# Kernel tuning notes

Hardware: AMD Instinct MI355X
Metric: run time of the kernel (lower is better)

The kernel has to match this reference:

```python
import jax, jax.numpy as jnp
import numpy as np

TOP_K = 2
CAP_FACTOR = 1.25


def _gelu(x):
    # custom tanh GELU matching the torch module
    return 0.5 * x * (1.0 + jnp.tanh(jnp.sqrt(2.0 / jnp.pi) * (x + 0.044715 * x ** 3)))


def setup_inputs() -> dict:
    key = jax.random.key(0)
    ks = jax.random.split(key, 6)
    B, S, D, F, E = 4, 2048, 1024, 4096, 8
    return {
        "hidden_states": jax.random.normal(ks[0], (B, S, D), dtype=jnp.float32),
        "wr": jax.random.normal(ks[1], (E, D), dtype=jnp.float32) * 0.02,  # router weight (Linear, no bias)
        "w1": jax.random.normal(ks[2], (E, D, F), dtype=jnp.float32) * 0.02,
        "b1": jnp.zeros((E, F), dtype=jnp.float32),
        "w2": jax.random.normal(ks[3], (E, F, D), dtype=jnp.float32) * 0.02,
        "b2": jnp.zeros((E, D), dtype=jnp.float32),
    }


def reference(hidden_states, wr, w1, b1, w2, b2):
    B, S, D = hidden_states.shape
    E = wr.shape[0]
    x = hidden_states.reshape(-1, D)  # [T, D]
    T = x.shape[0]

    # ---- router (eval mode: no noise) ----
    logits = x @ wr.T  # [T, E]
    vals, idx = jax.lax.top_k(logits, TOP_K)  # [T, K]
    sparse = jnp.full((T, E), -jnp.inf, dtype=logits.dtype)
    sparse = sparse.at[jnp.arange(T)[:, None], idx].set(vals)
    gating = jax.nn.softmax(sparse, axis=-1)  # [T, E], zero off top-k

    # ---- capacity-limited dispatch ----
    cap = max(8, int(max(1, T * TOP_K // E) * CAP_FACTOR))
    mask = (idx[:, :, None] == jnp.arange(E)).any(axis=1)  # [T, E]
    pos = jnp.cumsum(mask.astype(jnp.int32), axis=0) - 1  # rank of token within expert
    keep = mask & (pos < cap)
    slot = jnp.where(keep, pos, cap)  # overflow -> dummy slot
    e_grid = jnp.broadcast_to(jnp.arange(E)[None, :], (T, E))
    t_grid = jnp.broadcast_to(jnp.arange(T)[:, None], (T, E))
    dispatch = jnp.full((E, cap + 1), T, dtype=jnp.int32)
    dispatch = dispatch.at[e_grid, slot].set(t_grid)[:, :cap]  # [E, cap], T = pad

    # ---- grouped expert MLP ----
    x_pad = jnp.concatenate([x, jnp.zeros((1, D), x.dtype)], axis=0)
    g_pad = jnp.concatenate([gating, jnp.zeros((1, E), gating.dtype)], axis=0)
    xg = x_pad[dispatch]  # [E, cap, D]
    h = _gelu(jnp.einsum('ecd,edf->ecf', xg, w1) + b1[:, None, :])
    y = jnp.einsum('ecf,efd->ecd', h, w2) + b2[:, None, :]  # [E, cap, D]
    g = g_pad[dispatch, jnp.arange(E)[:, None]]  # [E, cap]; 0 for padded slots
    wy = y * g[..., None]

    # ---- combine (scatter-add) ----
    out = jax.ops.segment_sum(wy.reshape(-1, D), dispatch.reshape(-1), num_segments=T + 1)[:T]
    return out.reshape(B, S, D)
```

## Files before the change

### kernel.cpp

```cpp
#include <hip/hip_runtime.h>
#include <cstdint>
#include <cstddef>

#define T_TOK 8192
#define D_DIM 1024
#define F_DIM 4096
#define E_NUM 8
#define CAP   2560
#define BKS   32
#define MYB   20
#define LDSB  16384

typedef __attribute__((ext_vector_type(8))) short bf16x8;
typedef __attribute__((ext_vector_type(8))) unsigned short u16x8;
typedef __attribute__((ext_vector_type(4))) float f32x4;

typedef const __attribute__((address_space(1))) void* gas_ptr;
typedef __attribute__((address_space(3))) void* las_ptr;

__device__ __forceinline__ unsigned short f2bf(float f) {
  unsigned u = __float_as_uint(f);
  u += 0x7FFF + ((u >> 16) & 1);
  return (unsigned short)(u >> 16);
}

__device__ __forceinline__ float gelu_f(float x) {
  float u = 0.7978845608028654f * (x + 0.044715f * x * x * x);
  float t = 1.0f - 2.0f / (__expf(2.0f * u) + 1.0f);
  return 0.5f * x * (1.0f + t);
}

__device__ __forceinline__ int xcd_swizzle(int bid, int nwg) {
  int q = nwg >> 3;
  return (bid & 7) * q + (bid >> 3);
}

#define PIPE_BAR4() asm volatile("s_waitcnt vmcnt(4)\n\ts_barrier" ::: "memory")
#define PIPE_BAR0() asm volatile("s_waitcnt vmcnt(0)\n\ts_barrier" ::: "memory")

__global__ __launch_bounds__(256) void route_kernel(
    const float* __restrict__ x, const float* __restrict__ wr,
    unsigned short* __restrict__ xbf, int2* __restrict__ tokE,
    float2* __restrict__ tokG)
{
  int tid = threadIdx.x;
  int l = tid & 63;
  int w = tid >> 6;
  int t = blockIdx.x * 4 + w;
  const float4* xr = (const float4*)(x + (size_t)t * D_DIM);
  ushort4* xbr = (ushort4*)(xbf + (size_t)t * D_DIM);
  float acc[E_NUM];
#pragma unroll
  for (int e = 0; e < E_NUM; ++e) acc[e] = 0.f;
#pragma unroll
  for (int c = 0; c < D_DIM / 256; ++c) {
    float4 xv = xr[c * 64 + l];
    ushort4 bv;
    bv.x = f2bf(xv.x); bv.y = f2bf(xv.y); bv.z = f2bf(xv.z); bv.w = f2bf(xv.w);
    xbr[c * 64 + l] = bv;
#pragma unroll
    for (int e = 0; e < E_NUM; ++e) {
      float4 wv = ((const float4*)(wr + (size_t)e * D_DIM))[c * 64 + l];
      acc[e] += xv.x * wv.x + xv.y * wv.y + xv.z * wv.z + xv.w * wv.w;
    }
  }
#pragma unroll
  for (int e = 0; e < E_NUM; ++e) {
#pragma unroll
    for (int s = 32; s > 0; s >>= 1) acc[e] += __shfl_xor(acc[e], s);
  }
  if (l == 0) {
    int e1 = 0; float v1 = acc[0];
#pragma unroll
    for (int e = 1; e < E_NUM; ++e) if (acc[e] > v1) { v1 = acc[e]; e1 = e; }
    int e2 = -1; float v2 = -3.4e38f;
#pragma unroll
    for (int e = 0; e < E_NUM; ++e) if (e != e1 && acc[e] > v2) { v2 = acc[e]; e2 = e; }
    float s = __expf(v2 - v1);
    float g1 = 1.f / (1.f + s);
    tokE[t] = make_int2(e1, e2);
    tokG[t] = make_float2(g1, s * g1);
  }
}

__global__ __launch_bounds__(256) void scan_kernel(
    const int2* __restrict__ tokE, const float2* __restrict__ tokG,
    int* __restrict__ dispatch, float* __restrict__ sgate, int* __restrict__ cnt)
{
  int e = blockIdx.x;
  int tid = threadIdx.x;
  int l = tid & 63;
  int w = tid >> 6;
  __shared__ int wsum[4];
  int base = 0;
  for (int chunk = 0; chunk < T_TOK; chunk += 256) {
    int t = chunk + tid;
    int2 te = tokE[t];
    float2 tg = tokG[t];
    bool f1 = (te.x == e);
    bool f2 = (te.y == e);
    bool f = f1 || f2;
    unsigned long long m = __ballot(f);
    int rank = __popcll(m & ((1ull << l) - 1ull));
    if (l == 0) wsum[w] = __popcll(m);
    __syncthreads();
    int woff = 0;
#pragma unroll
    for (int i = 0; i < 4; ++i) if (i < w) woff += wsum[i];
    int tot = wsum[0] + wsum[1] + wsum[2] + wsum[3];
    int pos = base + woff + rank;
    if (f && pos < CAP) {
      dispatch[e * CAP + pos] = t;
      sgate[e * CAP + pos] = f1 ? tg.x : tg.y;
    }
    base += tot;
    __syncthreads();
  }
  int start = base < CAP ? base : CAP;
  for (int p = start + tid; p < CAP; p += 256) {
    dispatch[e * CAP + p] = T_TOK;
    sgate[e * CAP + p] = 0.f;
  }
  if (tid == 0) cnt[e] = base < CAP ? base : CAP;
}

__global__ __launch_bounds__(256) void transpose_kernel(
    const float* __restrict__ src, unsigned short* __restrict__ dst,
    int K, int N)
{
  const float* s = src + (size_t)blockIdx.z * K * N;
  unsigned short* d = dst + (size_t)blockIdx.z * K * N;
  __shared__ float tile[64][65];
  int n0 = blockIdx.x * 64;
  int k0 = blockIdx.y * 64;
  int tid = threadIdx.x;
  int r = tid >> 4;
  int c4 = (tid & 15) * 4;
#pragma unroll
  for (int i = 0; i < 4; ++i) {
    int row = r + i * 16;
    float4 v = *(const float4*)&s[(size_t)(k0 + row) * N + n0 + c4];
    tile[row][c4] = v.x; tile[row][c4 + 1] = v.y;
    tile[row][c4 + 2] = v.z; tile[row][c4 + 3] = v.w;
  }
  __syncthreads();
  int n = tid >> 2;
  int kg = tid & 3;
#pragma unroll
  for (int j = 0; j < 2; ++j) {
    int kc = kg * 2 + j;
    u16x8 o;
#pragma unroll
    for (int q = 0; q < 8; ++q) o[q] = f2bf(tile[kc * 8 + q][n]);
    *(u16x8*)&d[(size_t)(n0 + n) * K + k0 + kc * 8] = o;
  }
}


#define G1_NXB (F_DIM / 128)
__global__ __launch_bounds__(256, 3) void gemm1_kernel(
    const unsigned short* __restrict__ xbf,
    const unsigned short* __restrict__ w1t,
    const float* __restrict__ b1,
    const int* __restrict__ dispatch,
    const int* __restrict__ cnt,
    unsigned short* __restrict__ h,
    int e_base, size_t w1stride, size_t hstride)
{
  int wg = xcd_swizzle(blockIdx.x, gridDim.x);
  int my = wg % MYB;
  int p  = wg / MYB;
  int nx = p % G1_NXB;
  int ez = p / G1_NXB;
  int e = e_base + ez;
  int m0 = my * 128;
  if (m0 >= cnt[e]) return;
  const unsigned short* w1e = w1t + (size_t)ez * w1stride;
  unsigned short* he = h + (size_t)ez * hstride;
  int n0 = nx * 128;
  int tid = threadIdx.x;
  int l = tid & 63;
  int wid = tid >> 6;
  int wm = wid >> 1, wn = wid & 1;
  int lrow = l & 15, lhi = l >> 4;

  __shared__ __align__(16) char lds[3 * LDSB];

  const unsigned short* ag[2];
  const unsigned short* bg[2];
  int ldsA[2], ldsB[2];
#pragma unroll
  for (int j = 0; j < 2; ++j) {
    int chunk = wid * 2 + j;
    int U = chunk * 64 + l;
    int u = U ^ ((U >> 3) & 7);
    int row = u >> 2, s = u & 3;
    int tok = dispatch[e * CAP + m0 + row];
    ag[j] = xbf + (size_t)tok * D_DIM + s * 8;
    bg[j] = w1e + (size_t)(n0 + row) * D_DIM + s * 8;
    ldsA[j] = chunk * 1024;
    ldsB[j] = 8192 + chunk * 1024;
  }

  int aoff[4], boff[4];
#pragma unroll
  for (int m = 0; m < 4; ++m) {
    int row = wm * 64 + m * 16 + lrow;
    int u = row * 4 + lhi;
    aoff[m] = (u ^ ((row >> 1) & 7)) * 16;
    int colr = wn * 64 + m * 16 + lrow;
    int ub = colr * 4 + lhi;
    boff[m] = 8192 + (ub ^ ((colr >> 1) & 7)) * 16;
  }

  f32x4 acc[4][4];
#pragma unroll
  for (int m = 0; m < 4; ++m)
#pragma unroll
    for (int n = 0; n < 4; ++n) acc[m][n] = (f32x4){0.f, 0.f, 0.f, 0.f};

#define STAGE1(BASE, KOFF) do { \
    __builtin_amdgcn_global_load_lds((gas_ptr)(ag[0] + (KOFF)), (las_ptr)(lds + (BASE) + ldsA[0]), 16, 0, 0); \
    __builtin_amdgcn_global_load_lds((gas_ptr)(bg[0] + (KOFF)), (las_ptr)(lds + (BASE) + ldsB[0]), 16, 0, 0); \
    __builtin_amdgcn_global_load_lds((gas_ptr)(ag[1] + (KOFF)), (las_ptr)(lds + (BASE) + ldsA[1]), 16, 0, 0); \
    __builtin_amdgcn_global_load_lds((gas_ptr)(bg[1] + (KOFF)), (las_ptr)(lds + (BASE) + ldsB[1]), 16, 0, 0); \
  } while (0)

  const int NT = D_DIM / BKS;
  STAGE1(0, 0);
  STAGE1(LDSB, BKS);
  PIPE_BAR4();

  int cb = 0, sb = 2 * LDSB, koff = 2 * BKS;
  for (int t = 0; t < NT; ++t) {
    if (t + 2 < NT) { STAGE1(sb, koff); koff += BKS; }
    bf16x8 af[4], bfr[4];
#pragma unroll
    for (int m = 0; m < 4; ++m) af[m] = *(const bf16x8*)(lds + cb + aoff[m]);
#pragma unroll
    for (int n = 0; n < 4; ++n) bfr[n] = *(const bf16x8*)(lds + cb + boff[n]);
    __builtin_amdgcn_s_setprio(1);
#pragma unroll
    for (int m = 0; m < 4; ++m)
#pragma unroll
      for (int n = 0; n < 4; ++n)
        acc[m][n] = __builtin_amdgcn_mfma_f32_16x16x32_bf16(af[m], bfr[n], acc[m][n], 0, 0, 0);
    __builtin_amdgcn_s_setprio(0);
    if (t + 1 < NT) {
      if (t + 2 < NT) PIPE_BAR4(); else PIPE_BAR0();
      cb = (cb == 2 * LDSB) ? 0 : cb + LDSB;
      sb = (sb == 2 * LDSB) ? 0 : sb + LDSB;
    }
  }

  int colg[4]; float b1v[4];
#pragma unroll
  for (int n = 0; n < 4; ++n) {
    colg[n] = n0 + wn * 64 + n * 16 + lrow;
    b1v[n] = b1[e * F_DIM + colg[n]];
  }
#pragma unroll
  for (int m = 0; m < 4; ++m) {
    int rb = m0 + wm * 64 + m * 16 + lhi * 4;
#pragma unroll
    for (int j = 0; j < 4; ++j) {
      int r = rb + j;
      unsigned short* hr = he + (size_t)r * F_DIM;
#pragma unroll
      for (int n = 0; n < 4; ++n) {
        float v = acc[m][n][j] + b1v[n];
        hr[colg[n]] = f2bf(gelu_f(v));
      }
    }
  }
}

#define G2_NXB (D_DIM / 128)
__global__ __launch_bounds__(256, 3) void gemm2_kernel(
    const unsigned short* __restrict__ h,
    const unsigned short* __restrict__ w2t,
    const float* __restrict__ b2,
    const int* __restrict__ dispatch,
    const float* __restrict__ sgate,
    const int* __restrict__ cnt,
    float* __restrict__ out,
    int e_base, size_t w2stride, size_t hstride)
{
  int wg = xcd_swizzle(blockIdx.x, gridDim.x);
  int my = wg % MYB;
  int p  = wg / MYB;
  int nx = p % G2_NXB;
  int ez = p / G2_NXB;
  int e = e_base + ez;
  int m0 = my * 128;
  if (m0 >= cnt[e]) return;
  const unsigned short* he = h + (size_t)ez * hstride;
  const unsigned short* w2e = w2t + (size_t)ez * w2stride;
  int n0 = nx * 128;
  int tid = threadIdx.x;
  int l = tid & 63;
  int wid = tid >> 6;
  int wm = wid >> 1, wn = wid & 1;
  int lrow = l & 15, lhi = l >> 4;

  __shared__ __align__(16) char lds[3 * LDSB];

  const unsigned short* ag[2];
  const unsigned short* bg[2];
  int ldsA[2], ldsB[2];
#pragma unroll
  for (int j = 0; j < 2; ++j) {
    int chunk = wid * 2 + j;
    int U = chunk * 64 + l;
    int u = U ^ ((U >> 3) & 7);
    int row = u >> 2, s = u & 3;
    ag[j] = he + (size_t)(m0 + row) * F_DIM + s * 8;
    bg[j] = w2e + (size_t)(n0 + row) * F_DIM + s * 8;
    ldsA[j] = chunk * 1024;
    ldsB[j] = 8192 + chunk * 1024;
  }

  int aoff[4], boff[4];
#pragma unroll
  for (int m = 0; m < 4; ++m) {
    int row = wm * 64 + m * 16 + lrow;
    int u = row * 4 + lhi;
    aoff[m] = (u ^ ((row >> 1) & 7)) * 16;
    int colr = wn * 64 + m * 16 + lrow;
    int ub = colr * 4 + lhi;
    boff[m] = 8192 + (ub ^ ((colr >> 1) & 7)) * 16;
  }

  f32x4 acc[4][4];
#pragma unroll
  for (int m = 0; m < 4; ++m)
#pragma unroll
    for (int n = 0; n < 4; ++n) acc[m][n] = (f32x4){0.f, 0.f, 0.f, 0.f};

#define STAGE2(BASE, KOFF) do { \
    __builtin_amdgcn_global_load_lds((gas_ptr)(ag[0] + (KOFF)), (las_ptr)(lds + (BASE) + ldsA[0]), 16, 0, 0); \
    __builtin_amdgcn_global_load_lds((gas_ptr)(bg[0] + (KOFF)), (las_ptr)(lds + (BASE) + ldsB[0]), 16, 0, 0); \
    __builtin_amdgcn_global_load_lds((gas_ptr)(ag[1] + (KOFF)), (las_ptr)(lds + (BASE) + ldsA[1]), 16, 0, 0); \
    __builtin_amdgcn_global_load_lds((gas_ptr)(bg[1] + (KOFF)), (las_ptr)(lds + (BASE) + ldsB[1]), 16, 0, 0); \
  } while (0)

  const int NT = F_DIM / BKS;
  STAGE2(0, 0);
  STAGE2(LDSB, BKS);
  PIPE_BAR4();

  int cb = 0, sb = 2 * LDSB, koff = 2 * BKS;
  for (int t = 0; t < NT; ++t) {
    if (t + 2 < NT) { STAGE2(sb, koff); koff += BKS; }
    bf16x8 af[4], bfr[4];
#pragma unroll
    for (int m = 0; m < 4; ++m) af[m] = *(const bf16x8*)(lds + cb + aoff[m]);
#pragma unroll
    for (int n = 0; n < 4; ++n) bfr[n] = *(const bf16x8*)(lds + cb + boff[n]);
    __builtin_amdgcn_s_setprio(1);
#pragma unroll
    for (int m = 0; m < 4; ++m)
#pragma unroll
      for (int n = 0; n < 4; ++n)
        acc[m][n] = __builtin_amdgcn_mfma_f32_16x16x32_bf16(af[m], bfr[n], acc[m][n], 0, 0, 0);
    __builtin_amdgcn_s_setprio(0);
    if (t + 1 < NT) {
      if (t + 2 < NT) PIPE_BAR4(); else PIPE_BAR0();
      cb = (cb == 2 * LDSB) ? 0 : cb + LDSB;
      sb = (sb == 2 * LDSB) ? 0 : sb + LDSB;
    }
  }

  int colg[4]; float b2v[4];
#pragma unroll
  for (int n = 0; n < 4; ++n) {
    colg[n] = n0 + wn * 64 + n * 16 + lrow;
    b2v[n] = b2[e * D_DIM + colg[n]];
  }
#pragma unroll
  for (int m = 0; m < 4; ++m) {
    int rb = m0 + wm * 64 + m * 16 + lhi * 4;
#pragma unroll
    for (int j = 0; j < 4; ++j) {
      int r = rb + j;
      int tok = dispatch[e * CAP + r];
      if (tok < T_TOK) {
        float g = sgate[e * CAP + r];
        float* orow = out + (size_t)tok * D_DIM;
#pragma unroll
        for (int n = 0; n < 4; ++n)
          atomicAdd(&orow[colg[n]], g * (acc[m][n][j] + b2v[n]));
      }
    }
  }
}

extern "C" void kernel_launch(void* const* d_in, const int* in_sizes, int n_in,
                              void* d_out, int out_size, void* d_ws, size_t ws_size,
                              hipStream_t stream) {
  const float* x  = (const float*)d_in[0];
  const float* wr = (const float*)d_in[1];
  const float* w1 = (const float*)d_in[2];
  const float* b1 = (const float*)d_in[3];
  const float* w2 = (const float*)d_in[4];
  const float* b2 = (const float*)d_in[5];
  float* out = (float*)d_out;

  char* ws = (char*)d_ws;
  size_t off = 0;
  auto alloc = [&](size_t bytes) -> void* {
    off = (off + 255) & ~(size_t)255;
    void* p = ws + off;
    off += bytes;
    return p;
  };
  int*   dispatch = (int*)alloc((size_t)E_NUM * CAP * 4);
  float* sgate    = (float*)alloc((size_t)E_NUM * CAP * 4);
  int*   cnt      = (int*)alloc((size_t)E_NUM * 4);
  int2*  tokE     = (int2*)alloc((size_t)T_TOK * 8);
  float2* tokG    = (float2*)alloc((size_t)T_TOK * 8);
  unsigned short* xbf = (unsigned short*)alloc((size_t)(T_TOK + 1) * D_DIM * 2);

  const size_t wsz = (size_t)D_DIM * F_DIM * 2;
  const size_t hsz = (size_t)CAP * F_DIM * 2;
  size_t remain = ws_size > off ? ws_size - off : 0;
  bool tierA = remain >= (size_t)E_NUM * (2 * wsz + hsz) + (size_t)(1 << 16);

  hipMemsetAsync(out, 0, (size_t)T_TOK * D_DIM * 4, stream);
  hipMemsetAsync(xbf + (size_t)T_TOK * D_DIM, 0, D_DIM * 2, stream);
  route_kernel<<<T_TOK / 4, 256, 0, stream>>>(x, wr, xbf, tokE, tokG);
  scan_kernel<<<E_NUM, 256, 0, stream>>>(tokE, tokG, dispatch, sgate, cnt);

  if (tierA) {
    unsigned short* w1t = (unsigned short*)alloc((size_t)E_NUM * wsz);
    unsigned short* w2t = (unsigned short*)alloc((size_t)E_NUM * wsz);
    unsigned short* hb  = (unsigned short*)alloc((size_t)E_NUM * hsz);
    transpose_kernel<<<dim3(F_DIM / 64, D_DIM / 64, E_NUM), 256, 0, stream>>>(w1, w1t, D_DIM, F_DIM);
    transpose_kernel<<<dim3(D_DIM / 64, F_DIM / 64, E_NUM), 256, 0, stream>>>(w2, w2t, F_DIM, D_DIM);
    gemm1_kernel<<<dim3(G1_NXB * MYB * E_NUM), 256, 0, stream>>>(
        xbf, w1t, b1, dispatch, cnt, hb, 0, wsz / 2, hsz / 2);
    gemm2_kernel<<<dim3(G2_NXB * MYB * E_NUM), 256, 0, stream>>>(
        hb, w2t, b2, dispatch, sgate, cnt, out, 0, wsz / 2, hsz / 2);
  } else {
    unsigned short* w1t = (unsigned short*)alloc(wsz);
    unsigned short* w2t = (unsigned short*)alloc(wsz);
    unsigned short* hb  = (unsigned short*)alloc(hsz);
    for (int e = 0; e < E_NUM; ++e) {
      transpose_kernel<<<dim3(F_DIM / 64, D_DIM / 64, 1), 256, 0, stream>>>(
          w1 + (size_t)e * D_DIM * F_DIM, w1t, D_DIM, F_DIM);
      gemm1_kernel<<<dim3(G1_NXB * MYB), 256, 0, stream>>>(
          xbf, w1t, b1, dispatch, cnt, hb, e, 0, 0);
      transpose_kernel<<<dim3(D_DIM / 64, F_DIM / 64, 1), 256, 0, stream>>>(
          w2 + (size_t)e * D_DIM * F_DIM, w2t, F_DIM, D_DIM);
      gemm2_kernel<<<dim3(G2_NXB * MYB), 256, 0, stream>>>(
          hb, w2t, b2, dispatch, sgate, cnt, out, e, 0, 0);
    }
  }
}
```

Baseline: 774.0 us.

## Use 256x128 tiles with BK=64, 512 threads, and compact expert block scheduling

Grows the GEMM tile from 128x128 to 256x128 with a K-step of 64 and 512 threads (8 waves), and splits each K tile into two half-steps so loads overlap with MFMA. A small plan kernel computes a prefix sum of per-expert 256-row block counts, so the grid only launches blocks for real work instead of early-exiting empty capacity tiles. This raises data reuse per LDS byte and cuts wasted blocks. In exchange it uses 144KB of LDS per block, adds an extra launch, and puts more barriers in the inner loop.

```diff
diff --git a/kernel.cpp b/kernel.cpp
--- a/kernel.cpp
+++ b/kernel.cpp
@@ -7,9 +7,10 @@
 #define F_DIM 4096
 #define E_NUM 8
 #define CAP   2560
-#define BKS   32
-#define MYB   20
-#define LDSB  16384
+#define NWMAX 80
+#define NXB1  (F_DIM / 128)
+#define NXB2  (D_DIM / 128)
+#define BUFB  49152
 
 typedef __attribute__((ext_vector_type(8))) short bf16x8;
 typedef __attribute__((ext_vector_type(8))) unsigned short u16x8;
@@ -29,14 +30,6 @@
   float t = 1.0f - 2.0f / (__expf(2.0f * u) + 1.0f);
   return 0.5f * x * (1.0f + t);
 }
-
-__device__ __forceinline__ int xcd_swizzle(int bid, int nwg) {
-  int q = nwg >> 3;
-  return (bid & 7) * q + (bid >> 3);
-}
-
-#define PIPE_BAR4() asm volatile("s_waitcnt vmcnt(4)\n\ts_barrier" ::: "memory")
-#define PIPE_BAR0() asm volatile("s_waitcnt vmcnt(0)\n\ts_barrier" ::: "memory")
 
 __global__ __launch_bounds__(256) void route_kernel(
     const float* __restrict__ x, const float* __restrict__ wr,
@@ -124,6 +117,16 @@
   if (tid == 0) cnt[e] = base < CAP ? base : CAP;
 }
 
+__global__ __launch_bounds__(64) void plan_kernel(
+    const int* __restrict__ cnt, int* __restrict__ pre)
+{
+  if (threadIdx.x == 0) {
+    int s = 0;
+    for (int e = 0; e < E_NUM; ++e) { pre[e] = s; s += (cnt[e] + 255) >> 8; }
+    pre[E_NUM] = s;
+  }
+}
+
 __global__ __launch_bounds__(256) void transpose_kernel(
     const float* __restrict__ src, unsigned short* __restrict__ dst,
     int K, int N)
@@ -157,239 +160,240 @@
 }
 
 
-#define G1_NXB (F_DIM / 128)
-__global__ __launch_bounds__(256, 3) void gemm1_kernel(
+__device__ __forceinline__ bool map_block(
+    const int* __restrict__ pre, int nxb, int eSel,
+    int& e, int& m0, int& nx)
+{
+  int W;
+  if (eSel >= 0) W = (pre[eSel + 1] - pre[eSel]) * nxb;
+  else W = pre[E_NUM] * nxb;
+  int W8 = (W + 7) & ~7;
+  if ((int)blockIdx.x >= W8) return false;
+  int q = W8 >> 3;
+  int wg = ((int)blockIdx.x & 7) * q + ((int)blockIdx.x >> 3);
+  if (wg >= W) return false;
+  if (eSel >= 0) {
+    e = eSel;
+    int mb = pre[eSel + 1] - pre[eSel];
+    nx = wg / mb; m0 = (wg % mb) << 8;
+  } else {
+    e = 0;
+#pragma unroll
+    for (int i = 1; i < E_NUM; ++i) if (wg >= pre[i] * nxb) e = i;
+    int local = wg - pre[e] * nxb;
+    int mb = pre[e + 1] - pre[e];
+    nx = local / mb; m0 = (local % mb) << 8;
+  }
+  return true;
+}
+
+#define GEMM_CORE(AKSTRIDE, NT, STGJ)                                          \
+  int tid = threadIdx.x;                                                       \
+  int lane = tid & 63;                                                         \
+  int wid = tid >> 6;                                                          \
+  int wm = wid >> 1, wn = wid & 1;                                             \
+  int lrow = lane & 15, lhi = lane >> 4;                                       \
+                                       \
+  int aoff[4][2], boff[4][2];                                                  \
+  _Pragma("unroll")                                                            \
+  for (int m = 0; m < 4; ++m) {                                                \
+    int row = wm * 64 + m * 16 + lrow;                                         \
+    _Pragma("unroll")                                                          \
+    for (int kk = 0; kk < 2; ++kk) {                                           \
+      int s = kk * 4 + lhi;                                                    \
+      aoff[m][kk] = row * 128 + ((s ^ (row & 7)) << 4);                        \
+    }                                                                          \
+  }                                                                            \
+  _Pragma("unroll")                                                            \
+  for (int n = 0; n < 4; ++n) {                                                \
+    int rowb = wn * 64 + n * 16 + lrow;                                        \
+    _Pragma("unroll")                                                          \
+    for (int kk = 0; kk < 2; ++kk) {                                           \
+      int s = kk * 4 + lhi;                                                    \
+      boff[n][kk] = 32768 + rowb * 128 + ((s ^ (rowb & 7)) << 4);              \
+    }                                                                          \
+  }                                                                            \
+  f32x4 acc[4][4];                                                             \
+  _Pragma("unroll")                                                            \
+  for (int m = 0; m < 4; ++m)                                                  \
+    _Pragma("unroll")                                                          \
+    for (int n = 0; n < 4; ++n) acc[m][n] = (f32x4){0.f, 0.f, 0.f, 0.f};       \
+                                        \
+  _Pragma("unroll")                                                            \
+  for (int j = 0; j < 6; ++j) STGJ(j, 0, 0);                                   \
+  _Pragma("unroll")                                                            \
+  for (int j = 0; j < 6; ++j) STGJ(j, 1, BUFB);                                \
+  asm volatile("s_waitcnt vmcnt(6)\n\ts_barrier" ::: "memory");                \
+  int cb = 0, nb = 2 * BUFB;                                                   \
+  _Pragma("unroll 1")                                                          \
+  for (int t = 0; t < NT; ++t) {                                               \
+    bf16x8 fa[4], fb[4];                                                       \
+                                               \
+    _Pragma("unroll")                                                          \
+    for (int m = 0; m < 4; ++m) fa[m] = *(const bf16x8*)(lds + cb + aoff[m][0]);\
+    _Pragma("unroll")                                                          \
+    for (int n = 0; n < 4; ++n) fb[n] = *(const bf16x8*)(lds + cb + boff[n][0]);\
+    if (t + 2 < NT) {                                                          \
+      STGJ(0, t + 2, nb); STGJ(1, t + 2, nb); STGJ(2, t + 2, nb);              \
+    }                                                                          \
+    __builtin_amdgcn_s_barrier();                                              \
+    __builtin_amdgcn_s_setprio(1);                                             \
+    _Pragma("unroll")                                                          \
+    for (int m = 0; m < 4; ++m)                                                \
+      _Pragma("unroll")                                                        \
+      for (int n = 0; n < 4; ++n)                                              \
+        acc[m][n] = __builtin_amdgcn_mfma_f32_16x16x32_bf16(fa[m], fb[n], acc[m][n], 0, 0, 0); \
+    __builtin_amdgcn_s_setprio(0);                                             \
+    __builtin_amdgcn_s_barrier();                                              \
+                                               \
+    _Pragma("unroll")                                                          \
+    for (int m = 0; m < 4; ++m) fa[m] = *(const bf16x8*)(lds + cb + aoff[m][1]);\
+    _Pragma("unroll")                                                          \
+    for (int n = 0; n < 4; ++n) fb[n] = *(const bf16x8*)(lds + cb + boff[n][1]);\
+    if (t + 2 < NT) {                                                          \
+      STGJ(3, t + 2, nb); STGJ(4, t + 2, nb); STGJ(5, t + 2, nb);              \
+    }                                                                          \
+    __builtin_amdgcn_s_barrier();                                              \
+    __builtin_amdgcn_s_setprio(1);                                             \
+    _Pragma("unroll")                                                          \
+    for (int m = 0; m < 4; ++m)                                                \
+      _Pragma("unroll")                                                        \
+      for (int n = 0; n < 4; ++n)                                              \
+        acc[m][n] = __builtin_amdgcn_mfma_f32_16x16x32_bf16(fa[m], fb[n], acc[m][n], 0, 0, 0); \
+    __builtin_amdgcn_s_setprio(0);                                             \
+    if (t + 1 < NT) {                                                          \
+      if (t + 2 < NT)                                                          \
+        asm volatile("s_waitcnt vmcnt(6)\n\ts_barrier" ::: "memory");          \
+      else                                                                     \
+        asm volatile("s_waitcnt vmcnt(0)\n\ts_barrier" ::: "memory");          \
+      cb = (cb == 2 * BUFB) ? 0 : cb + BUFB;                                   \
+      nb = (nb == 2 * BUFB) ? 0 : nb + BUFB;                                   \
+    }                                                                          \
+  }
+
+__global__ __launch_bounds__(512, 2) void gemm1_kernel(
     const unsigned short* __restrict__ xbf,
     const unsigned short* __restrict__ w1t,
     const float* __restrict__ b1,
     const int* __restrict__ dispatch,
-    const int* __restrict__ cnt,
+    const int* __restrict__ pre,
     unsigned short* __restrict__ h,
-    int e_base, size_t w1stride, size_t hstride)
-{
-  int wg = xcd_swizzle(blockIdx.x, gridDim.x);
-  int my = wg % MYB;
-  int p  = wg / MYB;
-  int nx = p % G1_NXB;
-  int ez = p / G1_NXB;
-  int e = e_base + ez;
-  int m0 = my * 128;
-  if (m0 >= cnt[e]) return;
-  const unsigned short* w1e = w1t + (size_t)ez * w1stride;
+    int eSel, size_t wstride, size_t hstride)
+{
+  int e, m0, nx;
+  if (!map_block(pre, NXB1, eSel, e, m0, nx)) return;
+  int ez = (eSel >= 0) ? 0 : e;
+  const unsigned short* w1e = w1t + (size_t)ez * wstride;
   unsigned short* he = h + (size_t)ez * hstride;
   int n0 = nx * 128;
-  int tid = threadIdx.x;
-  int l = tid & 63;
-  int wid = tid >> 6;
-  int wm = wid >> 1, wn = wid & 1;
-  int lrow = l & 15, lhi = l >> 4;
-
-  __shared__ __align__(16) char lds[3 * LDSB];
-
-  const unsigned short* ag[2];
-  const unsigned short* bg[2];
-  int ldsA[2], ldsB[2];
-#pragma unroll
-  for (int j = 0; j < 2; ++j) {
-    int chunk = wid * 2 + j;
-    int U = chunk * 64 + l;
-    int u = U ^ ((U >> 3) & 7);
-    int row = u >> 2, s = u & 3;
-    int tok = dispatch[e * CAP + m0 + row];
-    ag[j] = xbf + (size_t)tok * D_DIM + s * 8;
-    bg[j] = w1e + (size_t)(n0 + row) * D_DIM + s * 8;
-    ldsA[j] = chunk * 1024;
-    ldsB[j] = 8192 + chunk * 1024;
-  }
-
-  int aoff[4], boff[4];
-#pragma unroll
-  for (int m = 0; m < 4; ++m) {
-    int row = wm * 64 + m * 16 + lrow;
-    int u = row * 4 + lhi;
-    aoff[m] = (u ^ ((row >> 1) & 7)) * 16;
-    int colr = wn * 64 + m * 16 + lrow;
-    int ub = colr * 4 + lhi;
-    boff[m] = 8192 + (ub ^ ((colr >> 1) & 7)) * 16;
-  }
-
-  f32x4 acc[4][4];
-#pragma unroll
-  for (int m = 0; m < 4; ++m)
-#pragma unroll
-    for (int n = 0; n < 4; ++n) acc[m][n] = (f32x4){0.f, 0.f, 0.f, 0.f};
-
-#define STAGE1(BASE, KOFF) do { \
-    __builtin_amdgcn_global_load_lds((gas_ptr)(ag[0] + (KOFF)), (las_ptr)(lds + (BASE) + ldsA[0]), 16, 0, 0); \
-    __builtin_amdgcn_global_load_lds((gas_ptr)(bg[0] + (KOFF)), (las_ptr)(lds + (BASE) + ldsB[0]), 16, 0, 0); \
-    __builtin_amdgcn_global_load_lds((gas_ptr)(ag[1] + (KOFF)), (las_ptr)(lds + (BASE) + ldsA[1]), 16, 0, 0); \
-    __builtin_amdgcn_global_load_lds((gas_ptr)(bg[1] + (KOFF)), (las_ptr)(lds + (BASE) + ldsB[1]), 16, 0, 0); \
-  } while (0)
-
-  const int NT = D_DIM / BKS;
-  STAGE1(0, 0);
-  STAGE1(LDSB, BKS);
-  PIPE_BAR4();
-
-  int cb = 0, sb = 2 * LDSB, koff = 2 * BKS;
-  for (int t = 0; t < NT; ++t) {
-    if (t + 2 < NT) { STAGE1(sb, koff); koff += BKS; }
-    bf16x8 af[4], bfr[4];
-#pragma unroll
-    for (int m = 0; m < 4; ++m) af[m] = *(const bf16x8*)(lds + cb + aoff[m]);
-#pragma unroll
-    for (int n = 0; n < 4; ++n) bfr[n] = *(const bf16x8*)(lds + cb + boff[n]);
-    __builtin_amdgcn_s_setprio(1);
-#pragma unroll
-    for (int m = 0; m < 4; ++m)
-#pragma unroll
-      for (int n = 0; n < 4; ++n)
-        acc[m][n] = __builtin_amdgcn_mfma_f32_16x16x32_bf16(af[m], bfr[n], acc[m][n], 0, 0, 0);
-    __builtin_amdgcn_s_setprio(0);
-    if (t + 1 < NT) {
-      if (t + 2 < NT) PIPE_BAR4(); else PIPE_BAR0();
-      cb = (cb == 2 * LDSB) ? 0 : cb + LDSB;
-      sb = (sb == 2 * LDSB) ? 0 : sb + LDSB;
-    }
-  }
-
-  int colg[4]; float b1v[4];
+
+  __shared__ __align__(16) char lds[3 * BUFB];
+
+  const unsigned short* sp[6];
+  int sbase[6];
+  {
+    int lane_ = threadIdx.x & 63, wid_ = threadIdx.x >> 6;
+#pragma unroll
+    for (int j = 0; j < 6; ++j) {
+      int c = j >> 1;
+      int seg = wid_ * 2 + (j & 1);
+      int Uc = seg * 64 + lane_;
+      int rl = Uc >> 3, sl = Uc & 7;
+      int colblk = (sl ^ (rl & 7)) * 8;
+      if (c < 2) {
+        int tok = dispatch[e * CAP + m0 + c * 128 + rl];
+        sp[j] = xbf + (size_t)tok * D_DIM + colblk;
+      } else {
+        sp[j] = w1e + (size_t)(n0 + rl) * D_DIM + colblk;
+      }
+      sbase[j] = c * 16384 + seg * 1024;
+    }
+  }
+#define STG_1(J, TT, BB) __builtin_amdgcn_global_load_lds(                     \
+    (gas_ptr)(sp[J] + (TT) * 64), (las_ptr)(lds + (BB) + sbase[J]), 16, 0, 0)
+
+  GEMM_CORE(D_DIM, (D_DIM / 64), STG_1)
+
+  int colg[4]; float bv[4];
 #pragma unroll
   for (int n = 0; n < 4; ++n) {
     colg[n] = n0 + wn * 64 + n * 16 + lrow;
-    b1v[n] = b1[e * F_DIM + colg[n]];
+    bv[n] = b1[e * F_DIM + colg[n]];
   }
 #pragma unroll
   for (int m = 0; m < 4; ++m) {
-    int rb = m0 + wm * 64 + m * 16 + lhi * 4;
 #pragma unroll
     for (int j = 0; j < 4; ++j) {
-      int r = rb + j;
+      int r = m0 + wm * 64 + m * 16 + lhi * 4 + j;
       unsigned short* hr = he + (size_t)r * F_DIM;
 #pragma unroll
-      for (int n = 0; n < 4; ++n) {
-        float v = acc[m][n][j] + b1v[n];
-        hr[colg[n]] = f2bf(gelu_f(v));
-      }
-    }
-  }
-}
-
-#define G2_NXB (D_DIM / 128)
-__global__ __launch_bounds__(256, 3) void gemm2_kernel(
+      for (int n = 0; n < 4; ++n)
+        hr[colg[n]] = f2bf(gelu_f(acc[m][n][j] + bv[n]));
+    }
+  }
+}
+
+__global__ __launch_bounds__(512, 2) void gemm2_kernel(
     const unsigned short* __restrict__ h,
     const unsigned short* __restrict__ w2t,
     const float* __restrict__ b2,
     const int* __restrict__ dispatch,
     const float* __restrict__ sgate,
-    const int* __restrict__ cnt,
+    const int* __restrict__ pre,
     float* __restrict__ out,
-    int e_base, size_t w2stride, size_t hstride)
-{
-  int wg = xcd_swizzle(blockIdx.x, gridDim.x);
-  int my = wg % MYB;
-  int p  = wg / MYB;
-  int nx = p % G2_NXB;
-  int ez = p / G2_NXB;
-  int e = e_base + ez;
-  int m0 = my * 128;
-  if (m0 >= cnt[e]) return;
+    int eSel, size_t wstride, size_t hstride)
+{
+  int e, m0, nx;
+  if (!map_block(pre, NXB2, eSel, e, m0, nx)) return;
+  int ez = (eSel >= 0) ? 0 : e;
   const unsigned short* he = h + (size_t)ez * hstride;
-  const unsigned short* w2e = w2t + (size_t)ez * w2stride;
+  const unsigned short* w2e = w2t + (size_t)ez * wstride;
   int n0 = nx * 128;
-  int tid = threadIdx.x;
-  int l = tid & 63;
-  int wid = tid >> 6;
-  int wm = wid >> 1, wn = wid & 1;
-  int lrow = l & 15, lhi = l >> 4;
-
-  __shared__ __align__(16) char lds[3 * LDSB];
-
-  const unsigned short* ag[2];
-  const unsigned short* bg[2];
-  int ldsA[2], ldsB[2];
-#pragma unroll
-  for (int j = 0; j < 2; ++j) {
-    int chunk = wid * 2 + j;
-    int U = chunk * 64 + l;
-    int u = U ^ ((U >> 3) & 7);
-    int row = u >> 2, s = u & 3;
-    ag[j] = he + (size_t)(m0 + row) * F_DIM + s * 8;
-    bg[j] = w2e + (size_t)(n0 + row) * F_DIM + s * 8;
-    ldsA[j] = chunk * 1024;
-    ldsB[j] = 8192 + chunk * 1024;
-  }
-
-  int aoff[4], boff[4];
-#pragma unroll
-  for (int m = 0; m < 4; ++m) {
-    int row = wm * 64 + m * 16 + lrow;
-    int u = row * 4 + lhi;
-    aoff[m] = (u ^ ((row >> 1) & 7)) * 16;
-    int colr = wn * 64 + m * 16 + lrow;
-    int ub = colr * 4 + lhi;
-    boff[m] = 8192 + (ub ^ ((colr >> 1) & 7)) * 16;
-  }
-
-  f32x4 acc[4][4];
-#pragma unroll
-  for (int m = 0; m < 4; ++m)
-#pragma unroll
-    for (int n = 0; n < 4; ++n) acc[m][n] = (f32x4){0.f, 0.f, 0.f, 0.f};
-
-#define STAGE2(BASE, KOFF) do { \
-    __builtin_amdgcn_global_load_lds((gas_ptr)(ag[0] + (KOFF)), (las_ptr)(lds + (BASE) + ldsA[0]), 16, 0, 0); \
-    __builtin_amdgcn_global_load_lds((gas_ptr)(bg[0] + (KOFF)), (las_ptr)(lds + (BASE) + ldsB[0]), 16, 0, 0); \
-    __builtin_amdgcn_global_load_lds((gas_ptr)(ag[1] + (KOFF)), (las_ptr)(lds + (BASE) + ldsA[1]), 16, 0, 0); \
-    __builtin_amdgcn_global_load_lds((gas_ptr)(bg[1] + (KOFF)), (las_ptr)(lds + (BASE) + ldsB[1]), 16, 0, 0); \
-  } while (0)
-
-  const int NT = F_DIM / BKS;
-  STAGE2(0, 0);
-  STAGE2(LDSB, BKS);
-  PIPE_BAR4();
-
-  int cb = 0, sb = 2 * LDSB, koff = 2 * BKS;
-  for (int t = 0; t < NT; ++t) {
-    if (t + 2 < NT) { STAGE2(sb, koff); koff += BKS; }
-    bf16x8 af[4], bfr[4];
-#pragma unroll
-    for (int m = 0; m < 4; ++m) af[m] = *(const bf16x8*)(lds + cb + aoff[m]);
-#pragma unroll
-    for (int n = 0; n < 4; ++n) bfr[n] = *(const bf16x8*)(lds + cb + boff[n]);
-    __builtin_amdgcn_s_setprio(1);
-#pragma unroll
-    for (int m = 0; m < 4; ++m)
-#pragma unroll
-      for (int n = 0; n < 4; ++n)
-        acc[m][n] = __builtin_amdgcn_mfma_f32_16x16x32_bf16(af[m], bfr[n], acc[m][n], 0, 0, 0);
-    __builtin_amdgcn_s_setprio(0);
-    if (t + 1 < NT) {
-      if (t + 2 < NT) PIPE_BAR4(); else PIPE_BAR0();
-      cb = (cb == 2 * LDSB) ? 0 : cb + LDSB;
-      sb = (sb == 2 * LDSB) ? 0 : sb + LDSB;
-    }
-  }
-
-  int colg[4]; float b2v[4];
+
+  __shared__ __align__(16) char lds[3 * BUFB];
+
+  const unsigned short* sp[6];
+  int sbase[6];
+  {
+    int lane_ = threadIdx.x & 63, wid_ = threadIdx.x >> 6;
+#pragma unroll
+    for (int j = 0; j < 6; ++j) {
+      int c = j >> 1;
+      int seg = wid_ * 2 + (j & 1);
+      int Uc = seg * 64 + lane_;
+      int rl = Uc >> 3, sl = Uc & 7;
+      int colblk = (sl ^ (rl & 7)) * 8;
+      if (c < 2) {
+        sp[j] = he + (size_t)(m0 + c * 128 + rl) * F_DIM + colblk;
+      } else {
+        sp[j] = w2e + (size_t)(n0 + rl) * F_DIM + colblk;
+      }
+      sbase[j] = c * 16384 + seg * 1024;
+    }
+  }
+#define STG_2(J, TT, BB) __builtin_amdgcn_global_load_lds(                     \
+    (gas_ptr)(sp[J] + (TT) * 64), (las_ptr)(lds + (BB) + sbase[J]), 16, 0, 0)
+
+  GEMM_CORE(F_DIM, (F_DIM / 64), STG_2)
+
+  int colg[4]; float bv[4];
 #pragma unroll
   for (int n = 0; n < 4; ++n) {
     colg[n] = n0 + wn * 64 + n * 16 + lrow;
-    b2v[n] = b2[e * D_DIM + colg[n]];
+    bv[n] = b2[e * D_DIM + colg[n]];
   }
 #pragma unroll
   for (int m = 0; m < 4; ++m) {
-    int rb = m0 + wm * 64 + m * 16 + lhi * 4;
 #pragma unroll
     for (int j = 0; j < 4; ++j) {
-      int r = rb + j;
+      int r = m0 + wm * 64 + m * 16 + lhi * 4 + j;
       int tok = dispatch[e * CAP + r];
       if (tok < T_TOK) {
         float g = sgate[e * CAP + r];
         float* orow = out + (size_t)tok * D_DIM;
 #pragma unroll
         for (int n = 0; n < 4; ++n)
-          atomicAdd(&orow[colg[n]], g * (acc[m][n][j] + b2v[n]));
+          atomicAdd(&orow[colg[n]], g * (acc[m][n][j] + bv[n]));
       }
     }
   }
@@ -417,6 +421,7 @@
   int*   dispatch = (int*)alloc((size_t)E_NUM * CAP * 4);
   float* sgate    = (float*)alloc((size_t)E_NUM * CAP * 4);
   int*   cnt      = (int*)alloc((size_t)E_NUM * 4);
+  int*   pre      = (int*)alloc((size_t)(E_NUM + 1) * 4);
   int2*  tokE     = (int2*)alloc((size_t)T_TOK * 8);
   float2* tokG    = (float2*)alloc((size_t)T_TOK * 8);
   unsigned short* xbf = (unsigned short*)alloc((size_t)(T_TOK + 1) * D_DIM * 2);
@@ -430,6 +435,7 @@
   hipMemsetAsync(xbf + (size_t)T_TOK * D_DIM, 0, D_DIM * 2, stream);
   route_kernel<<<T_TOK / 4, 256, 0, stream>>>(x, wr, xbf, tokE, tokG);
   scan_kernel<<<E_NUM, 256, 0, stream>>>(tokE, tokG, dispatch, sgate, cnt);
+  plan_kernel<<<1, 64, 0, stream>>>(cnt, pre);
 
   if (tierA) {
     unsigned short* w1t = (unsigned short*)alloc((size_t)E_NUM * wsz);
@@ -437,10 +443,10 @@
     unsigned short* hb  = (unsigned short*)alloc((size_t)E_NUM * hsz);
     transpose_kernel<<<dim3(F_DIM / 64, D_DIM / 64, E_NUM), 256, 0, stream>>>(w1, w1t, D_DIM, F_DIM);
     transpose_kernel<<<dim3(D_DIM / 64, F_DIM / 64, E_NUM), 256, 0, stream>>>(w2, w2t, F_DIM, D_DIM);
-    gemm1_kernel<<<dim3(G1_NXB * MYB * E_NUM), 256, 0, stream>>>(
-        xbf, w1t, b1, dispatch, cnt, hb, 0, wsz / 2, hsz / 2);
-    gemm2_kernel<<<dim3(G2_NXB * MYB * E_NUM), 256, 0, stream>>>(
-        hb, w2t, b2, dispatch, sgate, cnt, out, 0, wsz / 2, hsz / 2);
+    gemm1_kernel<<<dim3(NWMAX * NXB1), 512, 0, stream>>>(
+        xbf, w1t, b1, dispatch, pre, hb, -1, wsz / 2, hsz / 2);
+    gemm2_kernel<<<dim3(NWMAX * NXB2), 512, 0, stream>>>(
+        hb, w2t, b2, dispatch, sgate, pre, out, -1, wsz / 2, hsz / 2);
   } else {
     unsigned short* w1t = (unsigned short*)alloc(wsz);
     unsigned short* w2t = (unsigned short*)alloc(wsz);
@@ -448,12 +454,12 @@
     for (int e = 0; e < E_NUM; ++e) {
       transpose_kernel<<<dim3(F_DIM / 64, D_DIM / 64, 1), 256, 0, stream>>>(
           w1 + (size_t)e * D_DIM * F_DIM, w1t, D_DIM, F_DIM);
-      gemm1_kernel<<<dim3(G1_NXB * MYB), 256, 0, stream>>>(
-          xbf, w1t, b1, dispatch, cnt, hb, e, 0, 0);
+      gemm1_kernel<<<dim3((CAP / 256) * NXB1), 512, 0, stream>>>(
+          xbf, w1t, b1, dispatch, pre, hb, e, 0, 0);
       transpose_kernel<<<dim3(D_DIM / 64, F_DIM / 64, 1), 256, 0, stream>>>(
           w2 + (size_t)e * D_DIM * F_DIM, w2t, F_DIM, D_DIM);
-      gemm2_kernel<<<dim3(G2_NXB * MYB), 256, 0, stream>>>(
-          hb, w2t, b2, dispatch, sgate, cnt, out, e, 0, 0);
-    }
-  }
-}
+      gemm2_kernel<<<dim3((CAP / 256) * NXB2), 512, 0, stream>>>(
+          hb, w2t, b2, dispatch, sgate, pre, out, e, 0, 0);
+    }
+  }
+}
```

New measurement: 806.7 us. 4.2% more time.
